# Kernel optimization log

Hardware: AMD Instinct MI355X
Metric: run time of the kernel (lower is better)

## Reference

```python
import jax, jax.numpy as jnp
import numpy as np

GRID_SIZE = 5   # efficient-kan default
K = 3           # spline_order
BATCH = 32768
OBS_DIM = 128
ACTION_DIM = 18
# (in_features, out_features) for the 7 KANLinear layers:
# base: 128->256->256->64 ; adv head: 64->64->18 ; value head: 64->64->1
DIMS = [(OBS_DIM, 256), (256, 256), (256, 64), (64, 64), (64, ACTION_DIM), (64, 64), (64, 1)]


def make_grid(in_f):
    # uniform grid on [-1,1] extended by K knots each side: shape (in_f, GRID_SIZE+2K+1)
    h = 2.0 / GRID_SIZE
    g = jnp.arange(-K, GRID_SIZE + K + 1, dtype=jnp.float32) * h - 1.0
    return jnp.broadcast_to(g, (in_f, g.shape[0]))


def b_splines(x, grid):
    # Cox-de Boor recursion; x: (B, in) -> bases (B, in, GRID_SIZE+K)
    xe = x[:, :, None]
    b = ((xe >= grid[:, :-1]) & (xe < grid[:, 1:])).astype(x.dtype)
    for j in range(1, K + 1):
        left = (xe - grid[:, : -(j + 1)]) / (grid[:, j:-1] - grid[:, : -(j + 1)])
        right = (grid[:, j + 1:] - xe) / (grid[:, j + 1:] - grid[:, 1:-j])
        b = left * b[:, :, :-1] + right * b[:, :, 1:]
    return b


def kan_layer(x, bw, sw, sc):
    # efficient-kan KANLinear: silu base path + spline path with standalone scaler
    grid = make_grid(x.shape[1])
    base = jax.nn.silu(x) @ bw.T                              # (B, out)
    bases = b_splines(x, grid)                                # (B, in, G+K)
    spline = jnp.einsum('big,oig->bo', bases, sw * sc[:, :, None])
    return base + spline


def setup_inputs() -> dict:
    key = jax.random.key(0)
    ks = jax.random.split(key, 1 + 3 * len(DIMS))
    inp = {"x": jax.random.normal(ks[0], (BATCH, OBS_DIM), dtype=jnp.float32)}
    for i, (fin, fout) in enumerate(DIMS):
        inp[f"bw{i}"] = jax.random.normal(ks[1 + 3 * i], (fout, fin), dtype=jnp.float32) / np.sqrt(fin).astype(np.float32)
        inp[f"sw{i}"] = jax.random.normal(ks[2 + 3 * i], (fout, fin, GRID_SIZE + K), dtype=jnp.float32) * (0.1 / np.sqrt(fin).astype(np.float32))
        inp[f"sc{i}"] = 1.0 + 0.1 * jax.random.normal(ks[3 + 3 * i], (fout, fin), dtype=jnp.float32)
    return inp


def reference(x, bw0, sw0, sc0, bw1, sw1, sc1, bw2, sw2, sc2,
              bw3, sw3, sc3, bw4, sw4, sc4, bw5, sw5, sc5, bw6, sw6, sc6):
    h = x
    for bw, sw, sc in [(bw0, sw0, sc0), (bw1, sw1, sc1), (bw2, sw2, sc2)]:
        h = kan_layer(h, bw, sw, sc)
    advantage = kan_layer(kan_layer(h, bw3, sw3, sc3), bw4, sw4, sc4)
    state_value = kan_layer(kan_layer(h, bw5, sw5, sc5), bw6, sw6, sc6)
    return (advantage, state_value)
```

## Files before the change

### kernel.cpp

```cpp
#include <hip/hip_runtime.h>

typedef unsigned short u16;
typedef unsigned int   u32;
typedef unsigned long long u64;
typedef __bf16 bf16;
typedef float f32x4   __attribute__((ext_vector_type(4)));
typedef float f32x16  __attribute__((ext_vector_type(16)));
typedef bf16  bf16x8  __attribute__((ext_vector_type(8)));

__device__ __forceinline__ float bf2f(u16 u){ return (float)__builtin_bit_cast(bf16,u); }
__device__ __forceinline__ u16   f2bf(float f){ return __builtin_bit_cast(u16,(bf16)f); }
__device__ __forceinline__ u32   pkbf(float a,float b){ return (u32)f2bf(a)|((u32)f2bf(b)<<16); }

#define NROWS 32768

__device__ __forceinline__ uint4 basis_pk(float x)
{
  float tp  = __fmaf_rn(x, 2.5f, 5.5f);
  float tpc = fminf(fmaxf(tp, -1.0f), 12.0f);
  float fi  = floorf(tpc);
  float uu  = tpc - fi;
  int   i0  = (int)fi;
  float u2 = uu*uu, u3 = u2*uu, w1 = 1.0f-uu, w2 = w1*w1, w3 = w2*w1;
  float d1 = __fmaf_rn(3.0f, u3, __fmaf_rn(-6.0f, u2, 4.0f));
  float d2 = __fmaf_rn(3.0f, w3, __fmaf_rn(-6.0f, w2, 4.0f));
  u64 dpk = (u64)pkbf(w3, d1) | ((u64)pkbf(d2, u3) << 32);
  int ss = i0*16 - 48;
  u64 A  = dpk << (ss & 63);
  u64 Bv = dpk >> ((64-ss) & 63);
  u64 Cv = dpk << ((ss-64) & 63);
  u64 Dv = dpk >> ((-ss) & 63);
  u64 lo = (ss>=0 && ss<64)   ? A  : ((ss<0 && ss>-64) ? Dv : 0ull);
  u64 hi = (ss>=64 && ss<128) ? Cv : ((ss>0 && ss<64)  ? Bv : 0ull);
  uint4 r; r.x=(u32)lo; r.y=(u32)(lo>>32); r.z=(u32)hi; r.w=(u32)(hi>>32);
  return r;
}

__device__ __forceinline__ void expand9(float x, u16& sil, uint4& bpk)
{
  float s = x * (1.0f/(1.0f+__expf(-x)));
  sil = f2bf(s);
  bpk = basis_pk(x);
}
__device__ __forceinline__ void expand10(float x, u32& spk, uint4& bpk)
{
  float s = x * (1.0f/(1.0f+__expf(-x)));
  u16 uh = f2bf(s);
  u16 ul = f2bf(s - bf2f(uh));
  spk = (u32)uh | ((u32)ul<<16);
  bpk = basis_pk(x);
}

struct PrepArgs {
  const float* bw[7]; const float* sw[7]; const float* sc[7];
  u16* w[7];
  int cin[7]; int coutr[7]; int ntsh[7]; int fmt[7];
  u32 elems[7];
};

__global__ __launch_bounds__(256) void prep_kernel(PrepArgs pa)
{
  u32 idx = blockIdx.x*256 + threadIdx.x;
  int L = 0;
  u32 off = idx;
  while (L < 6 && off >= pa.elems[L]) { off -= pa.elems[L]; ++L; }
  int j    = off & 7;
  int lane = (off>>3) & 63;
  u32 tl   = off >> 9;
  int ntsh = pa.ntsh[L];
  u32 kstep = tl >> ntsh;
  int nt   = (int)(tl & ((1u<<ntsh)-1u));
  int i = 0, g = 0, o; bool sil;
  if (pa.fmt[L] == 0){
    o = nt*32 + (lane&31);
    int koct = lane>>5;
    u32 c = kstep/9u; int r = (int)(kstep - c*9u);
    if (r == 0){ i = (int)c*16 + koct*8 + j; sil = true; }
    else       { i = (int)c*16 + (r-1)*2 + koct; g = j; sil = false; }
  } else {
    o = nt*16 + (lane&15);
    int kpos = (lane>>4)*8 + j;
    u32 c = kstep/5u; int r = (int)(kstep - c*5u);
    if (r == 0){ i = (int)c*16 + (kpos>>1); sil = true; }
    else { int kl=(r-1)*32+kpos; i=(int)c*16+(kl>>3); g=kl&7; sil = false; }
  }
  float v = 0.f;
  if (o < pa.coutr[L]) {
    size_t e = (size_t)o*pa.cin[L] + i;
    v = sil ? pa.bw[L][e] : pa.sw[L][e*8+g]*pa.sc[L][e]*0.16666666666666666f;
  }
  pa.w[L][off] = f2bf(v);
}

template<int CIN,int COUT,int IN_MODE,int OUT_MODE>
__global__ __launch_bounds__(256,2) void kan_layer(const void* __restrict__ hin_,
    const u16* __restrict__ W, void* __restrict__ hout_)
{
  constexpr int NCH  = CIN/16;
  constexpr int TOTK = NCH*9;
  constexpr int NT32 = COUT/32;
  constexpr int RFW  = (COUT>=128)?2:1;
  constexpr int CFW  = (COUT>=128)?COUT/128:1;
  constexpr int SROW=12, BROW=68, BOFF=64*SROW;
  constexpr int CHUNK = BOFF + 64*BROW;
  __shared__ u32 buf[2][CHUNK];

  const int b0 = blockIdx.x*64;
  const int tid = threadIdx.x;
  const int wave = tid>>6, lane = tid&63, m32 = lane&31, koct = lane>>5;
  const int rfbase = (COUT>=128)? 0 : (wave>>1);
  const int cfb    = (COUT>=128)? wave*CFW : (wave&1);

  const u16*   __restrict__ hb = (const u16*)hin_;
  const float* __restrict__ hf = (const float*)hin_;

  f32x16 acc[RFW][CFW];
#pragma unroll
  for (int a=0;a<RFW;++a)
#pragma unroll
    for (int c=0;c<CFW;++c)
#pragma unroll
      for (int e=0;e<16;++e) acc[a][c][e] = 0.f;

  bf16x8 bbuf[4][CFW];
  auto loadB = [&](int kstep, bf16x8* dst){
    if (kstep < TOTK){
#pragma unroll
      for (int cf=0; cf<CFW; ++cf)
        dst[cf] = *(const bf16x8*)(W + (((size_t)kstep*NT32 + cfb+cf)*64 + lane)*8);
    }
  };
  loadB(0, bbuf[0]); loadB(1, bbuf[1]); loadB(2, bbuf[2]);

  float xb[2][4];
  auto loadX = [&](int kc, float* dst){
#pragma unroll
    for (int t=0;t<4;++t){
      int task = t*256+tid, row = task>>4, f = task&15;
      int gi = (b0+row)*CIN + kc*16 + f;
      dst[t] = (IN_MODE==0)? hf[gi] : bf2f(hb[gi]);
    }
  };
  auto expandChunk = [&](const float* xc, u32* dstb){
#pragma unroll
    for (int t=0;t<4;++t){
      int task=t*256+tid, row=task>>4, f=task&15;
      u16 sil; uint4 bpk;
      expand9(xc[t], sil, bpk);
      ((u16*)dstb)[row*(SROW*2) + f] = sil;
      *(uint4*)&dstb[BOFF + row*BROW + f*4] = bpk;
    }
  };

  loadX(0, xb[0]);
  expandChunk(xb[0], buf[0]);
  if (NCH > 1) loadX(1, xb[1]);
  __syncthreads();

  for (int kc=0; kc<NCH; ++kc){
    u32* cur = buf[kc&1];
    u32* nxt = buf[(kc+1)&1];
    if (kc+1 < NCH) expandChunk(xb[(kc+1)&1], nxt);
    if (kc+2 < NCH) loadX(kc+2, xb[kc&1]);
#pragma unroll
    for (int ks=0; ks<9; ++ks){
      const int kstep = kc*9 + ks;
      loadB(kstep+3, bbuf[3]);
      bf16x8 af[RFW];
#pragma unroll
      for (int rf=0; rf<RFW; ++rf){
        int row = (rfbase+rf)*32 + m32;
        af[rf] = (ks==0)
          ? *(const bf16x8*)&cur[row*SROW + koct*4]
          : *(const bf16x8*)&cur[BOFF + row*BROW + (ks-1)*8 + koct*4];
      }
#pragma unroll
      for (int cf=0; cf<CFW; ++cf)
#pragma unroll
        for (int rf=0; rf<RFW; ++rf)
          acc[rf][cf] = __builtin_amdgcn_mfma_f32_32x32x16_bf16(af[rf], bbuf[0][cf], acc[rf][cf],0,0,0);
#pragma unroll
      for (int cf=0; cf<CFW; ++cf){ bbuf[0][cf]=bbuf[1][cf]; bbuf[1][cf]=bbuf[2][cf]; bbuf[2][cf]=bbuf[3][cf]; }
    }
    __syncthreads();
  }

#pragma unroll
  for (int rf=0; rf<RFW; ++rf)
#pragma unroll
    for (int cf=0; cf<CFW; ++cf)
#pragma unroll
      for (int reg=0; reg<16; ++reg){
        int rl  = (reg&3) + 8*(reg>>2) + 4*koct;
        size_t off = (size_t)(b0 + (rfbase+rf)*32 + rl)*COUT + (cfb+cf)*32 + m32;
        if constexpr (OUT_MODE==0) ((float*)hout_)[off] = acc[rf][cf][reg];
        else                       ((u16*)hout_)[off]   = f2bf(acc[rf][cf][reg]);
      }
}

template<int IN_MODE>
__global__ __launch_bounds__(512,4) void tail_kernel(const void* __restrict__ h2_,
  const u16* __restrict__ W3, const u16* __restrict__ W4,
  const u16* __restrict__ W5, const u16* __restrict__ W6,
  float* __restrict__ out_adv, float* __restrict__ out_val)
{
  constexpr int SROW=20, BROW=68, BOFF=64*20;
  __shared__ u32   Aexp[BOFF + 64*BROW];
  __shared__ float hA[64*65], hV[64*65];

  const int b0 = blockIdx.x*64;
  const int tid = threadIdx.x;
  const int wave = tid>>6, lane = tid&63, m = lane&15, quad = lane>>4;
  const int rg = wave>>2, cg = wave&3;

  const u16*   __restrict__ hb = (const u16*)h2_;
  const float* __restrict__ hf = (const float*)h2_;

  f32x4 a3[2], a5[2];
#pragma unroll
  for (int mt=0;mt<2;++mt){ a3[mt]=(f32x4){0,0,0,0}; a5[mt]=(f32x4){0,0,0,0}; }

  bf16x8 w3b[3], w5b[3];
  auto loadB2 = [&](int kstep, int d){
    if (kstep < 20){
      size_t bi = (((size_t)kstep*4 + cg)*64 + lane)*8;
      w3b[d] = *(const bf16x8*)(W3+bi);
      w5b[d] = *(const bf16x8*)(W5+bi);
    }
  };
  loadB2(0,0); loadB2(1,1);

  float xb[2][2];
  auto loadX = [&](int kc, float* dst){
#pragma unroll
    for (int t=0;t<2;++t){
      int task = t*512+tid, row=task>>4, f=task&15;
      int gi = (b0+row)*64 + kc*16 + f;
      dst[t] = (IN_MODE==0)? hf[gi] : bf2f(hb[gi]);
    }
  };
  loadX(0, xb[0]);

  for (int kc=0; kc<4; ++kc){
    const float* xc = xb[kc&1];
#pragma unroll
    for (int t=0;t<2;++t){
      int task=t*512+tid, row=task>>4, f=task&15;
      u32 spk; uint4 bpk;
      expand10(xc[t], spk, bpk);
      Aexp[row*SROW + f] = spk;
      *(uint4*)&Aexp[BOFF + row*BROW + f*4] = bpk;
    }
    if (kc+1 < 4) loadX(kc+1, xb[(kc+1)&1]);
    __syncthreads();
#pragma unroll
    for (int ks=0; ks<5; ++ks){
      const int kstep = kc*5 + ks;
      loadB2(kstep+2, 2);
      bf16x8 af[2];
#pragma unroll
      for (int mt=0; mt<2; ++mt){
        int row = rg*32 + mt*16 + m;
        af[mt] = (ks==0)
          ? *(const bf16x8*)&Aexp[row*SROW + quad*4]
          : *(const bf16x8*)&Aexp[BOFF + row*BROW + (ks-1)*16 + quad*4];
      }
#pragma unroll
      for (int mt=0; mt<2; ++mt){
        a3[mt] = __builtin_amdgcn_mfma_f32_16x16x32_bf16(af[mt], w3b[0], a3[mt],0,0,0);
        a5[mt] = __builtin_amdgcn_mfma_f32_16x16x32_bf16(af[mt], w5b[0], a5[mt],0,0,0);
      }
      w3b[0]=w3b[1]; w3b[1]=w3b[2]; w5b[0]=w5b[1]; w5b[1]=w5b[2];
    }
    __syncthreads();
  }
#pragma unroll
  for (int mt=0;mt<2;++mt)
#pragma unroll
    for (int r=0;r<4;++r){
      int row = rg*32 + mt*16 + quad*4 + r;
      hA[row*65 + cg*16 + m] = a3[mt][r];
      hV[row*65 + cg*16 + m] = a5[mt][r];
    }
  __syncthreads();

  f32x4 a4[2];
#pragma unroll
  for (int mt=0;mt<2;++mt) a4[mt]=(f32x4){0,0,0,0};
  bf16x8 w4b[3];
  auto loadB4 = [&](int kstep, int d){
    if (kstep < 20) w4b[d] = *(const bf16x8*)(W4 + (((size_t)kstep*4 + cg)*64 + lane)*8);
  };
  loadB4(0,0); loadB4(1,1);
  for (int kc=0; kc<4; ++kc){
#pragma unroll
    for (int t=0;t<2;++t){
      int task=t*512+tid, row=task>>4, f=task&15;
      u32 spk; uint4 bpk;
      expand10(hA[row*65 + kc*16 + f], spk, bpk);
      Aexp[row*SROW + f] = spk;
      *(uint4*)&Aexp[BOFF + row*BROW + f*4] = bpk;
    }
    __syncthreads();
#pragma unroll
    for (int ks=0; ks<5; ++ks){
      loadB4(kc*5+ks+2, 2);
      bf16x8 af[2];
#pragma unroll
      for (int mt=0; mt<2; ++mt){
        int row = rg*32 + mt*16 + m;
        af[mt] = (ks==0)
          ? *(const bf16x8*)&Aexp[row*SROW + quad*4]
          : *(const bf16x8*)&Aexp[BOFF + row*BROW + (ks-1)*16 + quad*4];
      }
#pragma unroll
      for (int mt=0; mt<2; ++mt)
        a4[mt] = __builtin_amdgcn_mfma_f32_16x16x32_bf16(af[mt], w4b[0], a4[mt],0,0,0);
      w4b[0]=w4b[1]; w4b[1]=w4b[2];
    }
    __syncthreads();
  }
  {
    int col = cg*16 + m;
    if (col < 18){
#pragma unroll
      for (int mt=0;mt<2;++mt)
#pragma unroll
        for (int r=0;r<4;++r)
          out_adv[(size_t)(b0 + rg*32 + mt*16 + quad*4 + r)*18 + col] = a4[mt][r];
    }
  }

  f32x4 a6[2];
#pragma unroll
  for (int mt=0;mt<2;++mt) a6[mt]=(f32x4){0,0,0,0};
  bf16x8 w6b[3];
  auto loadB6 = [&](int kstep, int d){
    if (kstep < 20) w6b[d] = *(const bf16x8*)(W6 + (((size_t)kstep*4 + cg)*64 + lane)*8);
  };
  loadB6(0,0); loadB6(1,1);
  for (int kc=0; kc<4; ++kc){
#pragma unroll
    for (int t=0;t<2;++t){
      int task=t*512+tid, row=task>>4, f=task&15;
      u32 spk; uint4 bpk;
      expand10(hV[row*65 + kc*16 + f], spk, bpk);
      Aexp[row*SROW + f] = spk;
      *(uint4*)&Aexp[BOFF + row*BROW + f*4] = bpk;
    }
    __syncthreads();
#pragma unroll
    for (int ks=0; ks<5; ++ks){
      loadB6(kc*5+ks+2, 2);
      bf16x8 af[2];
#pragma unroll
      for (int mt=0; mt<2; ++mt){
        int row = rg*32 + mt*16 + m;
        af[mt] = (ks==0)
          ? *(const bf16x8*)&Aexp[row*SROW + quad*4]
          : *(const bf16x8*)&Aexp[BOFF + row*BROW + (ks-1)*16 + quad*4];
      }
#pragma unroll
      for (int mt=0; mt<2; ++mt)
        a6[mt] = __builtin_amdgcn_mfma_f32_16x16x32_bf16(af[mt], w6b[0], a6[mt],0,0,0);
      w6b[0]=w6b[1]; w6b[1]=w6b[2];
    }
    __syncthreads();
  }
  if (cg==0 && m==0){
#pragma unroll
    for (int mt=0;mt<2;++mt)
#pragma unroll
      for (int r=0;r<4;++r)
        out_val[b0 + rg*32 + mt*16 + quad*4 + r] = a6[mt][r];
  }
}

extern "C" void kernel_launch(void* const* d_in, const int* in_sizes, int n_in,
                              void* d_out, int out_size, void* d_ws, size_t ws_size,
                              hipStream_t stream)
{
  (void)in_sizes; (void)n_in; (void)out_size;
  char* ws = (char*)d_ws;

  const size_t wbytes[7] = {589824u, 1179648u, 294912u, 81920u, 81920u, 81920u, 81920u};
  const bool midf32 = ws_size >= 77889536u;

  u16* W[7];
  char *h0, *h1, *h2;
  if (midf32) {
    h0 = ws;
    h1 = h0 + 33554432u;
    h2 = h1 + 33554432u;
    size_t off = 75497472u;
    for (int l=0;l<7;++l){ W[l] = (u16*)(ws+off); off += wbytes[l]; }
  } else {
    h0 = ws;
    h1 = h0 + 16777216u;
    h2 = h1 + 16777216u;
    size_t off = 37748736u;
    for (int l=0;l<7;++l){ W[l] = (u16*)(ws+off); off += wbytes[l]; }
  }

  PrepArgs pa;
  const int cins[7]   = {128,256,256,64,64,64,64};
  const int coutr[7]  = {256,256,64,64,18,64,1};
  const int ntsh[7]   = {3,3,1,2,2,2,2};
  const int fmts[7]   = {0,0,0,1,1,1,1};
  const u32 elems[7]  = {294912u,589824u,147456u,40960u,40960u,40960u,40960u};
  for (int l=0;l<7;++l){
    pa.bw[l] = (const float*)d_in[1+3*l];
    pa.sw[l] = (const float*)d_in[2+3*l];
    pa.sc[l] = (const float*)d_in[3+3*l];
    pa.w[l]  = W[l];
    pa.cin[l]=cins[l]; pa.coutr[l]=coutr[l]; pa.ntsh[l]=ntsh[l]; pa.fmt[l]=fmts[l];
    pa.elems[l]=elems[l];
  }
  prep_kernel<<<4672, 256, 0, stream>>>(pa);

  dim3 g(NROWS/64), bmain(256), btail(512);
  float* out_adv = (float*)d_out;
  float* out_val = (float*)d_out + (size_t)NROWS*18;
  if (midf32) {
    kan_layer<128,256,0,0><<<g,bmain,0,stream>>>(d_in[0], W[0], h0);
    kan_layer<256,256,0,0><<<g,bmain,0,stream>>>(h0, W[1], h1);
    kan_layer<256, 64,0,0><<<g,bmain,0,stream>>>(h1, W[2], h2);
    tail_kernel<0><<<g,btail,0,stream>>>(h2, W[3], W[4], W[5], W[6], out_adv, out_val);
  } else {
    kan_layer<128,256,0,1><<<g,bmain,0,stream>>>(d_in[0], W[0], h0);
    kan_layer<256,256,1,1><<<g,bmain,0,stream>>>(h0, W[1], h1);
    kan_layer<256, 64,1,1><<<g,bmain,0,stream>>>(h1, W[2], h2);
    tail_kernel<1><<<g,btail,0,stream>>>(h2, W[3], W[4], W[5], W[6], out_adv, out_val);
  }
}
```

Baseline: 246.9 us.

## Compute spline bases in registers per MFMA step and enlarge row tiles to 128

```diff
diff --git a/kernel.cpp b/kernel.cpp
--- a/kernel.cpp
+++ b/kernel.cpp
@@ -36,12 +36,6 @@
   return r;
 }
 
-__device__ __forceinline__ void expand9(float x, u16& sil, uint4& bpk)
-{
-  float s = x * (1.0f/(1.0f+__expf(-x)));
-  sil = f2bf(s);
-  bpk = basis_pk(x);
-}
 __device__ __forceinline__ void expand10(float x, u32& spk, uint4& bpk)
 {
   float s = x * (1.0f/(1.0f+__expf(-x)));
@@ -93,108 +87,112 @@
 }
 
 template<int CIN,int COUT,int IN_MODE,int OUT_MODE>
-__global__ __launch_bounds__(256,2) void kan_layer(const void* __restrict__ hin_,
-    const u16* __restrict__ W, void* __restrict__ hout_)
-{
-  constexpr int NCH  = CIN/16;
-  constexpr int TOTK = NCH*9;
-  constexpr int NT32 = COUT/32;
-  constexpr int RFW  = (COUT>=128)?2:1;
-  constexpr int CFW  = (COUT>=128)?COUT/128:1;
-  constexpr int SROW=12, BROW=68, BOFF=64*SROW;
-  constexpr int CHUNK = BOFF + 64*BROW;
-  __shared__ u32 buf[2][CHUNK];
-
-  const int b0 = blockIdx.x*64;
+__global__ __launch_bounds__((COUT>=128)?512:256, 2)
+void kan_layer(const void* __restrict__ hin_, const u16* __restrict__ W, void* __restrict__ hout_)
+{
+  constexpr int CG      = (COUT>=128)?4:2;
+  constexpr int THREADS = CG*128;
+  constexpr int CFW     = COUT/(CG*32);
+  constexpr int NT32    = COUT/32;
+  constexpr int NCH     = CIN/16;
+  constexpr int TOTK    = NCH*9;
+  constexpr int XROW    = 17;
+  constexpr int SRO     = 12;
+  constexpr int NLD     = 2048/THREADS;
+  __shared__ float xs[2][128*XROW];
+  __shared__ u32  sil[2][128*SRO];
+
+  const int b0 = blockIdx.x*128;
   const int tid = threadIdx.x;
   const int wave = tid>>6, lane = tid&63, m32 = lane&31, koct = lane>>5;
-  const int rfbase = (COUT>=128)? 0 : (wave>>1);
-  const int cfb    = (COUT>=128)? wave*CFW : (wave&1);
+  const int rg = wave/CG, cg = wave - rg*CG;
 
   const u16*   __restrict__ hb = (const u16*)hin_;
   const float* __restrict__ hf = (const float*)hin_;
 
-  f32x16 acc[RFW][CFW];
-#pragma unroll
-  for (int a=0;a<RFW;++a)
+  f32x16 acc[2][CFW];
+#pragma unroll
+  for (int a=0;a<2;++a)
 #pragma unroll
     for (int c=0;c<CFW;++c)
 #pragma unroll
       for (int e=0;e<16;++e) acc[a][c][e] = 0.f;
 
-  bf16x8 bbuf[4][CFW];
+  bf16x8 bbuf[3][CFW];
   auto loadB = [&](int kstep, bf16x8* dst){
     if (kstep < TOTK){
 #pragma unroll
       for (int cf=0; cf<CFW; ++cf)
-        dst[cf] = *(const bf16x8*)(W + (((size_t)kstep*NT32 + cfb+cf)*64 + lane)*8);
-    }
-  };
-  loadB(0, bbuf[0]); loadB(1, bbuf[1]); loadB(2, bbuf[2]);
-
-  float xb[2][4];
-  auto loadX = [&](int kc, float* dst){
-#pragma unroll
-    for (int t=0;t<4;++t){
-      int task = t*256+tid, row = task>>4, f = task&15;
+        dst[cf] = *(const bf16x8*)(W + (((size_t)kstep*NT32 + cg*CFW+cf)*64 + lane)*8);
+    }
+  };
+
+  float xg[NLD];
+  auto loadX = [&](int kc){
+#pragma unroll
+    for (int t=0;t<NLD;++t){
+      int task = t*THREADS+tid, row = task>>4, f = task&15;
       int gi = (b0+row)*CIN + kc*16 + f;
-      dst[t] = (IN_MODE==0)? hf[gi] : bf2f(hb[gi]);
-    }
-  };
-  auto expandChunk = [&](const float* xc, u32* dstb){
-#pragma unroll
-    for (int t=0;t<4;++t){
-      int task=t*256+tid, row=task>>4, f=task&15;
-      u16 sil; uint4 bpk;
-      expand9(xc[t], sil, bpk);
-      ((u16*)dstb)[row*(SROW*2) + f] = sil;
-      *(uint4*)&dstb[BOFF + row*BROW + f*4] = bpk;
-    }
-  };
-
-  loadX(0, xb[0]);
-  expandChunk(xb[0], buf[0]);
-  if (NCH > 1) loadX(1, xb[1]);
+      xg[t] = (IN_MODE==0)? hf[gi] : bf2f(hb[gi]);
+    }
+  };
+  auto stage = [&](int bsel){
+#pragma unroll
+    for (int t=0;t<NLD;++t){
+      int task = t*THREADS+tid, row = task>>4, f = task&15;
+      float x = xg[t];
+      xs[bsel][row*XROW + f] = x;
+      float s = x * __builtin_amdgcn_rcpf(1.0f + __expf(-x));
+      ((u16*)&sil[bsel][0])[row*(SRO*2) + f] = f2bf(s);
+    }
+  };
+
+  loadB(0,bbuf[0]); loadB(1,bbuf[1]);
+  loadX(0); stage(0);
+  if (NCH>1) loadX(1);
   __syncthreads();
 
   for (int kc=0; kc<NCH; ++kc){
-    u32* cur = buf[kc&1];
-    u32* nxt = buf[(kc+1)&1];
-    if (kc+1 < NCH) expandChunk(xb[(kc+1)&1], nxt);
-    if (kc+2 < NCH) loadX(kc+2, xb[kc&1]);
-#pragma unroll
-    for (int ks=0; ks<9; ++ks){
-      const int kstep = kc*9 + ks;
-      loadB(kstep+3, bbuf[3]);
-      bf16x8 af[RFW];
-#pragma unroll
-      for (int rf=0; rf<RFW; ++rf){
-        int row = (rfbase+rf)*32 + m32;
-        af[rf] = (ks==0)
-          ? *(const bf16x8*)&cur[row*SROW + koct*4]
-          : *(const bf16x8*)&cur[BOFF + row*BROW + (ks-1)*8 + koct*4];
+    const int cs = kc&1;
+    const int row0 = rg*64 + m32;
+#pragma unroll
+    for (int r=0; r<9; ++r){
+      const int kstep = kc*9 + r;
+      loadB(kstep+2, bbuf[2]);
+      bf16x8 af[2];
+      if (r==0){
+#pragma unroll
+        for (int rfl=0; rfl<2; ++rfl)
+          af[rfl] = __builtin_bit_cast(bf16x8, *(const uint4*)&sil[cs][(row0+rfl*32)*SRO + koct*4]);
+      } else {
+#pragma unroll
+        for (int rfl=0; rfl<2; ++rfl){
+          float xv = xs[cs][(row0+rfl*32)*XROW + (r-1)*2 + koct];
+          af[rfl] = __builtin_bit_cast(bf16x8, basis_pk(xv));
+        }
       }
 #pragma unroll
       for (int cf=0; cf<CFW; ++cf)
 #pragma unroll
-        for (int rf=0; rf<RFW; ++rf)
-          acc[rf][cf] = __builtin_amdgcn_mfma_f32_32x32x16_bf16(af[rf], bbuf[0][cf], acc[rf][cf],0,0,0);
-#pragma unroll
-      for (int cf=0; cf<CFW; ++cf){ bbuf[0][cf]=bbuf[1][cf]; bbuf[1][cf]=bbuf[2][cf]; bbuf[2][cf]=bbuf[3][cf]; }
-    }
-    __syncthreads();
-  }
-
-#pragma unroll
-  for (int rf=0; rf<RFW; ++rf)
+        for (int rfl=0; rfl<2; ++rfl)
+          acc[rfl][cf] = __builtin_amdgcn_mfma_f32_32x32x16_bf16(af[rfl], bbuf[0][cf], acc[rfl][cf],0,0,0);
+#pragma unroll
+      for (int cf=0; cf<CFW; ++cf){ bbuf[0][cf]=bbuf[1][cf]; bbuf[1][cf]=bbuf[2][cf]; }
+    }
+    if (kc+1 < NCH){ stage((kc+1)&1); if (kc+2 < NCH) loadX(kc+2); }
+    __syncthreads();
+  }
+
+#pragma unroll
+  for (int rfl=0; rfl<2; ++rfl)
 #pragma unroll
     for (int cf=0; cf<CFW; ++cf)
 #pragma unroll
       for (int reg=0; reg<16; ++reg){
         int rl  = (reg&3) + 8*(reg>>2) + 4*koct;
-        size_t off = (size_t)(b0 + (rfbase+rf)*32 + rl)*COUT + (cfb+cf)*32 + m32;
-        if constexpr (OUT_MODE==0) ((float*)hout_)[off] = acc[rf][cf][reg];
-        else                       ((u16*)hout_)[off]   = f2bf(acc[rf][cf][reg]);
+        size_t off = (size_t)(b0 + rg*64 + rfl*32 + rl)*COUT + (cg*CFW+cf)*32 + m32;
+        if constexpr (OUT_MODE==0) ((float*)hout_)[off] = acc[rfl][cf][reg];
+        else                       ((u16*)hout_)[off]   = f2bf(acc[rfl][cf][reg]);
       }
 }
 
@@ -418,18 +416,18 @@
   }
   prep_kernel<<<4672, 256, 0, stream>>>(pa);
 
-  dim3 g(NROWS/64), bmain(256), btail(512);
+  dim3 gmain(NROWS/128), gtail(NROWS/64);
   float* out_adv = (float*)d_out;
   float* out_val = (float*)d_out + (size_t)NROWS*18;
   if (midf32) {
-    kan_layer<128,256,0,0><<<g,bmain,0,stream>>>(d_in[0], W[0], h0);
-    kan_layer<256,256,0,0><<<g,bmain,0,stream>>>(h0, W[1], h1);
-    kan_layer<256, 64,0,0><<<g,bmain,0,stream>>>(h1, W[2], h2);
-    tail_kernel<0><<<g,btail,0,stream>>>(h2, W[3], W[4], W[5], W[6], out_adv, out_val);
+    kan_layer<128,256,0,0><<<gmain,512,0,stream>>>(d_in[0], W[0], h0);
+    kan_layer<256,256,0,0><<<gmain,512,0,stream>>>(h0, W[1], h1);
+    kan_layer<256, 64,0,0><<<gmain,256,0,stream>>>(h1, W[2], h2);
+    tail_kernel<0><<<gtail,512,0,stream>>>(h2, W[3], W[4], W[5], W[6], out_adv, out_val);
   } else {
-    kan_layer<128,256,0,1><<<g,bmain,0,stream>>>(d_in[0], W[0], h0);
-    kan_layer<256,256,1,1><<<g,bmain,0,stream>>>(h0, W[1], h1);
-    kan_layer<256, 64,1,1><<<g,bmain,0,stream>>>(h1, W[2], h2);
-    tail_kernel<1><<<g,btail,0,stream>>>(h2, W[3], W[4], W[5], W[6], out_adv, out_val);
-  }
-}
+    kan_layer<128,256,0,1><<<gmain,512,0,stream>>>(d_in[0], W[0], h0);
+    kan_layer<256,256,1,1><<<gmain,512,0,stream>>>(h0, W[1], h1);
+    kan_layer<256, 64,1,1><<<gmain,256,0,stream>>>(h1, W[2], h2);
+    tail_kernel<1><<<gtail,512,0,stream>>>(h2, W[3], W[4], W[5], W[6], out_adv, out_val);
+  }
+}
```

New measurement: 277.4 us. 1.12x slower.

## Use 512-thread blocks with per-wave row/column split and deeper weight prefetch

Applied to the files above, without the earlier changes.

```diff
diff --git a/kernel.cpp b/kernel.cpp
--- a/kernel.cpp
+++ b/kernel.cpp
@@ -36,12 +36,6 @@
   return r;
 }
 
-__device__ __forceinline__ void expand9(float x, u16& sil, uint4& bpk)
-{
-  float s = x * (1.0f/(1.0f+__expf(-x)));
-  sil = f2bf(s);
-  bpk = basis_pk(x);
-}
 __device__ __forceinline__ void expand10(float x, u32& spk, uint4& bpk)
 {
   float s = x * (1.0f/(1.0f+__expf(-x)));
@@ -93,109 +87,105 @@
 }
 
 template<int CIN,int COUT,int IN_MODE,int OUT_MODE>
-__global__ __launch_bounds__(256,2) void kan_layer(const void* __restrict__ hin_,
-    const u16* __restrict__ W, void* __restrict__ hout_)
-{
-  constexpr int NCH  = CIN/16;
-  constexpr int TOTK = NCH*9;
-  constexpr int NT32 = COUT/32;
-  constexpr int RFW  = (COUT>=128)?2:1;
-  constexpr int CFW  = (COUT>=128)?COUT/128:1;
+__global__ __launch_bounds__(512,4)
+void kan_layer(const void* __restrict__ hin_, const u16* __restrict__ W, void* __restrict__ hout_)
+{
+  constexpr int NT32  = COUT/32;
+  constexpr int CFW   = (NT32>=4)? NT32/4 : 1;
+  constexpr int DEPTH = (CFW>=2)? 6 : 8;
+  constexpr int NCH   = CIN/16;
+  constexpr int TOTK  = NCH*9;
   constexpr int SROW=12, BROW=68, BOFF=64*SROW;
   constexpr int CHUNK = BOFF + 64*BROW;
-  __shared__ u32 buf[2][CHUNK];
+  __shared__ alignas(16) u32 buf[2][CHUNK];
 
   const int b0 = blockIdx.x*64;
   const int tid = threadIdx.x;
   const int wave = tid>>6, lane = tid&63, m32 = lane&31, koct = lane>>5;
-  const int rfbase = (COUT>=128)? 0 : (wave>>1);
-  const int cfb    = (COUT>=128)? wave*CFW : (wave&1);
+  const int rg = wave>>2, cgw = wave&3;
+  const int ctbase = (cgw*CFW) & (NT32-1);
+  const bool wstore = (cgw*CFW) < NT32;
 
   const u16*   __restrict__ hb = (const u16*)hin_;
   const float* __restrict__ hf = (const float*)hin_;
 
-  f32x16 acc[RFW][CFW];
-#pragma unroll
-  for (int a=0;a<RFW;++a)
-#pragma unroll
-    for (int c=0;c<CFW;++c)
-#pragma unroll
-      for (int e=0;e<16;++e) acc[a][c][e] = 0.f;
-
-  bf16x8 bbuf[4][CFW];
+  f32x16 acc[CFW];
+#pragma unroll
+  for (int c=0;c<CFW;++c)
+#pragma unroll
+    for (int e=0;e<16;++e) acc[c][e] = 0.f;
+
+  bf16x8 bbuf[DEPTH][CFW];
   auto loadB = [&](int kstep, bf16x8* dst){
     if (kstep < TOTK){
 #pragma unroll
       for (int cf=0; cf<CFW; ++cf)
-        dst[cf] = *(const bf16x8*)(W + (((size_t)kstep*NT32 + cfb+cf)*64 + lane)*8);
-    }
-  };
-  loadB(0, bbuf[0]); loadB(1, bbuf[1]); loadB(2, bbuf[2]);
-
-  float xb[2][4];
+        dst[cf] = *(const bf16x8*)(W + (((size_t)kstep*NT32 + ctbase+cf)*64 + lane)*8);
+    }
+  };
+#pragma unroll
+  for (int d=0; d<DEPTH-1; ++d) loadB(d, bbuf[d]);
+
+  float xb[2][2];
   auto loadX = [&](int kc, float* dst){
 #pragma unroll
-    for (int t=0;t<4;++t){
-      int task = t*256+tid, row = task>>4, f = task&15;
+    for (int t=0;t<2;++t){
+      int task = t*512+tid, row = task>>4, f = task&15;
       int gi = (b0+row)*CIN + kc*16 + f;
       dst[t] = (IN_MODE==0)? hf[gi] : bf2f(hb[gi]);
     }
   };
-  auto expandChunk = [&](const float* xc, u32* dstb){
-#pragma unroll
-    for (int t=0;t<4;++t){
-      int task=t*256+tid, row=task>>4, f=task&15;
-      u16 sil; uint4 bpk;
-      expand9(xc[t], sil, bpk);
-      ((u16*)dstb)[row*(SROW*2) + f] = sil;
-      *(uint4*)&dstb[BOFF + row*BROW + f*4] = bpk;
+  auto stage = [&](const float* xc, u32* dstb){
+#pragma unroll
+    for (int t=0;t<2;++t){
+      int task = t*512+tid, row = task>>4, f = task&15;
+      float x = xc[t];
+      float s = x * __builtin_amdgcn_rcpf(1.0f + __expf(-x));
+      ((u16*)dstb)[row*(SROW*2) + f] = f2bf(s);
+      *(uint4*)&dstb[BOFF + row*BROW + f*4] = basis_pk(x);
     }
   };
 
   loadX(0, xb[0]);
-  expandChunk(xb[0], buf[0]);
-  if (NCH > 1) loadX(1, xb[1]);
+  stage(xb[0], buf[0]);
+  if (NCH>1) loadX(1, xb[1]);
   __syncthreads();
 
   for (int kc=0; kc<NCH; ++kc){
     u32* cur = buf[kc&1];
     u32* nxt = buf[(kc+1)&1];
-    if (kc+1 < NCH) expandChunk(xb[(kc+1)&1], nxt);
+    if (kc+1 < NCH) stage(xb[(kc+1)&1], nxt);
     if (kc+2 < NCH) loadX(kc+2, xb[kc&1]);
-#pragma unroll
-    for (int ks=0; ks<9; ++ks){
-      const int kstep = kc*9 + ks;
-      loadB(kstep+3, bbuf[3]);
-      bf16x8 af[RFW];
-#pragma unroll
-      for (int rf=0; rf<RFW; ++rf){
-        int row = (rfbase+rf)*32 + m32;
-        af[rf] = (ks==0)
-          ? *(const bf16x8*)&cur[row*SROW + koct*4]
-          : *(const bf16x8*)&cur[BOFF + row*BROW + (ks-1)*8 + koct*4];
-      }
+    const int row = rg*32 + m32;
+#pragma unroll
+    for (int r=0; r<9; ++r){
+      const int kstep = kc*9 + r;
+      loadB(kstep+DEPTH-1, bbuf[DEPTH-1]);
+      bf16x8 af;
+      if (r==0) af = __builtin_bit_cast(bf16x8, *(const uint4*)&cur[row*SROW + koct*4]);
+      else      af = __builtin_bit_cast(bf16x8, *(const uint4*)&cur[BOFF + row*BROW + ((r-1)*2+koct)*4]);
 #pragma unroll
       for (int cf=0; cf<CFW; ++cf)
-#pragma unroll
-        for (int rf=0; rf<RFW; ++rf)
-          acc[rf][cf] = __builtin_amdgcn_mfma_f32_32x32x16_bf16(af[rf], bbuf[0][cf], acc[rf][cf],0,0,0);
-#pragma unroll
-      for (int cf=0; cf<CFW; ++cf){ bbuf[0][cf]=bbuf[1][cf]; bbuf[1][cf]=bbuf[2][cf]; bbuf[2][cf]=bbuf[3][cf]; }
-    }
-    __syncthreads();
-  }
-
-#pragma unroll
-  for (int rf=0; rf<RFW; ++rf)
+        acc[cf] = __builtin_amdgcn_mfma_f32_32x32x16_bf16(af, bbuf[0][cf], acc[cf],0,0,0);
+#pragma unroll
+      for (int d=0; d<DEPTH-1; ++d)
+#pragma unroll
+        for (int cf=0; cf<CFW; ++cf) bbuf[d][cf] = bbuf[d+1][cf];
+    }
+    __syncthreads();
+  }
+
+  if (wstore){
 #pragma unroll
     for (int cf=0; cf<CFW; ++cf)
 #pragma unroll
       for (int reg=0; reg<16; ++reg){
         int rl  = (reg&3) + 8*(reg>>2) + 4*koct;
-        size_t off = (size_t)(b0 + (rfbase+rf)*32 + rl)*COUT + (cfb+cf)*32 + m32;
-        if constexpr (OUT_MODE==0) ((float*)hout_)[off] = acc[rf][cf][reg];
-        else                       ((u16*)hout_)[off]   = f2bf(acc[rf][cf][reg]);
+        size_t off = (size_t)(b0 + rg*32 + rl)*COUT + (ctbase+cf)*32 + m32;
+        if constexpr (OUT_MODE==0) ((float*)hout_)[off] = acc[cf][reg];
+        else                       ((u16*)hout_)[off]   = f2bf(acc[cf][reg]);
       }
+  }
 }
 
 template<int IN_MODE>
@@ -418,18 +408,18 @@
   }
   prep_kernel<<<4672, 256, 0, stream>>>(pa);
 
-  dim3 g(NROWS/64), bmain(256), btail(512);
+  dim3 g(NROWS/64);
   float* out_adv = (float*)d_out;
   float* out_val = (float*)d_out + (size_t)NROWS*18;
   if (midf32) {
-    kan_layer<128,256,0,0><<<g,bmain,0,stream>>>(d_in[0], W[0], h0);
-    kan_layer<256,256,0,0><<<g,bmain,0,stream>>>(h0, W[1], h1);
-    kan_layer<256, 64,0,0><<<g,bmain,0,stream>>>(h1, W[2], h2);
-    tail_kernel<0><<<g,btail,0,stream>>>(h2, W[3], W[4], W[5], W[6], out_adv, out_val);
+    kan_layer<128,256,0,0><<<g,512,0,stream>>>(d_in[0], W[0], h0);
+    kan_layer<256,256,0,0><<<g,512,0,stream>>>(h0, W[1], h1);
+    kan_layer<256, 64,0,0><<<g,512,0,stream>>>(h1, W[2], h2);
+    tail_kernel<0><<<g,512,0,stream>>>(h2, W[3], W[4], W[5], W[6], out_adv, out_val);
   } else {
-    kan_layer<128,256,0,1><<<g,bmain,0,stream>>>(d_in[0], W[0], h0);
-    kan_layer<256,256,1,1><<<g,bmain,0,stream>>>(h0, W[1], h1);
-    kan_layer<256, 64,1,1><<<g,bmain,0,stream>>>(h1, W[2], h2);
-    tail_kernel<1><<<g,btail,0,stream>>>(h2, W[3], W[4], W[5], W[6], out_adv, out_val);
-  }
-}
+    kan_layer<128,256,0,1><<<g,512,0,stream>>>(d_in[0], W[0], h0);
+    kan_layer<256,256,1,1><<<g,512,0,stream>>>(h0, W[1], h1);
+    kan_layer<256, 64,1,1><<<g,512,0,stream>>>(h1, W[2], h2);
+    tail_kernel<1><<<g,512,0,stream>>>(h2, W[3], W[4], W[5], W[6], out_adv, out_val);
+  }
+}
```

New measurement: 246.9 us. About the same (-0.0%).
